# Optimization experiments

Measured on AMD Instinct MI355X. Metric: run time of the kernel, lower is better.

## Reference

```python
import jax, jax.numpy as jnp
import numpy as np

EPS = 1e-5
HEADS = 4
C = 128
GROUPS = 32  # min(32, 128//4)
SR = 2
SCALE = (C // HEADS) ** -0.5


def group_norm(x, gamma, beta, groups=GROUPS, eps=EPS):
    N, Ch, H, W = x.shape
    xg = x.reshape(N, groups, Ch // groups, H, W)
    mu = xg.mean(axis=(2, 3, 4), keepdims=True)
    var = xg.var(axis=(2, 3, 4), keepdims=True)
    xg = (xg - mu) * jax.lax.rsqrt(var + eps)
    x = xg.reshape(N, Ch, H, W)
    return x * gamma[None, :, None, None] + beta[None, :, None, None]


def conv1x1(x, W, b):
    # x: [N,C,H,W], W: [Cout,Cin], b: [Cout]
    return jnp.einsum('nchw,oc->nohw', x, W) + b[None, :, None, None]


def avg_pool2(x):
    N, Ch, H, W = x.shape
    return x.reshape(N, Ch, H // SR, SR, W // SR, SR).mean(axis=(3, 5))


def to_heads(x):
    # [N,C,H,W] -> [N,h,HW,C//h]  (matches view(N,h,C/h,HW).permute(0,1,3,2))
    N, Ch, H, W = x.shape
    return x.reshape(N, HEADS, Ch // HEADS, H * W).transpose(0, 1, 3, 2)


def setup_inputs() -> dict:
    key = jax.random.key(0)
    ks = jax.random.split(key, 16)
    B, H, W = 8, 64, 64
    s = 1.0 / np.sqrt(C)
    inp = {
        'q_src': jax.random.normal(ks[0], (B, C, H, W), jnp.float32),
        'k_src': jax.random.normal(ks[1], (B, C, H, W), jnp.float32),
        'v_src': jax.random.normal(ks[2], (B, C, H, W), jnp.float32),
        'Wq': jax.random.normal(ks[3], (C, C), jnp.float32) * s,
        'bq': jnp.zeros((C,), jnp.float32),
        'Wk': jax.random.normal(ks[4], (C, C), jnp.float32) * s,
        'bk': jnp.zeros((C,), jnp.float32),
        'Wv': jax.random.normal(ks[5], (C, C), jnp.float32) * s,
        'bv': jnp.zeros((C,), jnp.float32),
        'Wp': jax.random.normal(ks[6], (C, C), jnp.float32) * s,
        'bp': jnp.zeros((C,), jnp.float32),
        'g_nq': jnp.ones((C,), jnp.float32), 'b_nq': jnp.zeros((C,), jnp.float32),
        'g_nk': jnp.ones((C,), jnp.float32), 'b_nk': jnp.zeros((C,), jnp.float32),
        'g_nv': jnp.ones((C,), jnp.float32), 'b_nv': jnp.zeros((C,), jnp.float32),
        'g_srk': jnp.ones((C,), jnp.float32), 'b_srk': jnp.zeros((C,), jnp.float32),
        'g_srv': jnp.ones((C,), jnp.float32), 'b_srv': jnp.zeros((C,), jnp.float32),
    }
    return inp


def reference(q_src, k_src, v_src, Wq, bq, Wk, bk, Wv, bv, Wp, bp,
              g_nq, b_nq, g_nk, b_nk, g_nv, b_nv, g_srk, b_srk, g_srv, b_srv):
    # Q path: GN -> 1x1 conv
    q = conv1x1(group_norm(q_src, g_nq, b_nq), Wq, bq)
    # K/V paths: SR (avgpool + GN) -> GN -> 1x1 conv
    k = conv1x1(group_norm(group_norm(avg_pool2(k_src), g_srk, b_srk), g_nk, b_nk), Wk, bk)
    v = conv1x1(group_norm(group_norm(avg_pool2(v_src), g_srv, b_srv), g_nv, b_nv), Wv, bv)

    N, Cq, Hq, Wq_ = q.shape
    qh, kh, vh = to_heads(q), to_heads(k), to_heads(v)  # [N,h,L,d]
    attn = jnp.einsum('nhqd,nhkd->nhqk', qh * SCALE, kh)  # [N,h,Lq,Lk]
    attn = jax.nn.softmax(attn, axis=-1)
    out = jnp.einsum('nhqk,nhkd->nhqd', attn, vh)  # [N,h,Lq,d]
    out = out.transpose(0, 1, 3, 2).reshape(N, Cq, Hq, Wq_)
    return conv1x1(out, Wp, bp)
```

## Files before the change

### kernel.cpp

```cpp
#include <hip/hip_runtime.h>

typedef __attribute__((ext_vector_type(8)))  short s8v;
typedef __attribute__((ext_vector_type(4)))  short s4v;
typedef __attribute__((ext_vector_type(16))) float f16v;
typedef __attribute__((ext_vector_type(2)))  int   i2v;
typedef __attribute__((ext_vector_type(2)))  float f2v;

__device__ __forceinline__ unsigned short f2bf(float f) {
  union { float f; unsigned u; } v; v.f = f;
  unsigned r = v.u + 0x7FFFu + ((v.u >> 16) & 1u);
  return (unsigned short)(r >> 16);
}
__device__ __forceinline__ float bf2f(unsigned short b) {
  return __uint_as_float((unsigned)b << 16);
}
__device__ __forceinline__ float fexp2(float x) {
#if __has_builtin(__builtin_amdgcn_exp2f)
  return __builtin_amdgcn_exp2f(x);
#else
  return exp2f(x);
#endif
}
__device__ __forceinline__ f2v mk2(float a, float b) { f2v r; r[0] = a; r[1] = b; return r; }

__device__ __forceinline__ void gn_stats_body(
    int blk, const float* __restrict__ x, const float* __restrict__ gamma,
    const float* __restrict__ beta, float* __restrict__ ab, float* sh)
{
  int n = blk >> 5, g = blk & 31;
  int t = threadIdx.x; int cl = t >> 6, lane = t & 63;
  const float4* x4 = (const float4*)(x + (size_t)(n * 128 + g * 4 + cl) * 4096);
  float s = 0.f, ss = 0.f;
  #pragma unroll
  for (int j = 0; j < 16; ++j) {
    float4 v = x4[lane + 64 * j];
    s  += v.x + v.y + v.z + v.w;
    ss += v.x * v.x + v.y * v.y + v.z * v.z + v.w * v.w;
  }
  #pragma unroll
  for (int m = 32; m >= 1; m >>= 1) { s += __shfl_xor(s, m); ss += __shfl_xor(ss, m); }
  if (lane == 0) { sh[cl] = s; sh[4 + cl] = ss; }
  __syncthreads();
  if (t < 4) {
    float mu = (sh[0] + sh[1] + sh[2] + sh[3]) * (1.f / 16384.f);
    float e  = (sh[4] + sh[5] + sh[6] + sh[7]) * (1.f / 16384.f);
    float r  = rsqrtf(e - mu * mu + 1e-5f);
    int c = g * 4 + t;
    float al = gamma[c] * r;
    ab[n * 128 + c] = al;
    ab[1024 + n * 128 + c] = beta[c] - mu * al;
  }
}

__device__ __forceinline__ void pool_aff_body(
    int blk, const float* __restrict__ x,
    const float* __restrict__ g1, const float* __restrict__ b1,
    const float* __restrict__ g2, const float* __restrict__ b2,
    float* __restrict__ pooled, float* __restrict__ ab, float* sh)
{
  int n = blk >> 5, g = blk & 31;
  int t = threadIdx.x; int cl = t >> 6, lane = t & 63;
  int c = g * 4 + cl;
  const float* xb = x + (size_t)(n * 128 + c) * 4096;
  float* pb = pooled + (size_t)(n * 128 + c) * 1024;
  float s = 0.f, ss = 0.f;
  #pragma unroll
  for (int j = 0; j < 8; ++j) {
    int pp = (lane + 64 * j) * 2;
    int py = pp >> 5, px2 = pp & 31;
    const float* r0 = xb + py * 128 + px2 * 2;
    float4 A = *(const float4*)r0;
    float4 B = *(const float4*)(r0 + 64);
    float v0 = 0.25f * (A.x + A.y + B.x + B.y);
    float v1 = 0.25f * (A.z + A.w + B.z + B.w);
    float2 wv; wv.x = v0; wv.y = v1;
    *(float2*)(pb + pp) = wv;
    s += v0 + v1; ss += v0 * v0 + v1 * v1;
  }
  #pragma unroll
  for (int m = 32; m >= 1; m >>= 1) { s += __shfl_xor(s, m); ss += __shfl_xor(ss, m); }
  if (lane == 0) { sh[cl] = s; sh[4 + cl] = ss; }
  __syncthreads();
  if (t < 4) {
    float mu1 = (sh[0] + sh[1] + sh[2] + sh[3]) * (1.f / 4096.f);
    float e1  = (sh[4] + sh[5] + sh[6] + sh[7]) * (1.f / 4096.f);
    float r1  = rsqrtf(e1 - mu1 * mu1 + 1e-5f);
    float mzs = 0.f, e2s = 0.f;
    #pragma unroll
    for (int cc = 0; cc < 4; ++cc) {
      int ch = g * 4 + cc;
      float a = r1 * g1[ch];
      float d = b1[ch] - mu1 * a;
      float m = sh[cc] * (1.f / 1024.f);
      float q = sh[4 + cc] * (1.f / 1024.f);
      mzs += a * m + d;
      e2s += a * a * q + 2.f * a * d * m + d * d;
    }
    float mu2 = 0.25f * mzs;
    float r2  = rsqrtf(0.25f * e2s - mu2 * mu2 + 1e-5f);
    int ch = g * 4 + t;
    float a = r1 * g1[ch];
    float d = b1[ch] - mu1 * a;
    ab[n * 128 + ch] = a * r2 * g2[ch];
    ab[1024 + n * 128 + ch] = (d - mu2) * r2 * g2[ch] + b2[ch];
  }
}

__device__ __forceinline__ void wsplit_body(
    int b, const float* __restrict__ W, unsigned short* __restrict__ whi,
    unsigned short* __restrict__ wlo)
{
  int idx = b * 256 + threadIdx.x;
  #pragma unroll
  for (int k = 0; k < 4; ++k) {
    int f = idx + k * 4096;
    int o = f >> 7, c = f & 127;
    float v = W[f];
    unsigned short hb = f2bf(v);
    unsigned short lb = f2bf(v - bf2f(hb));
    int cq = c >> 2;
    int adr = (o * 16 + ((cq >> 1) ^ (o & 7))) * 8 + (cq & 1) * 4 + (c & 3);
    whi[adr] = hb; wlo[adr] = lb;
  }
}

__global__ __launch_bounds__(256) void prep_k(
    const float* __restrict__ q_src, const float* __restrict__ g_nq, const float* __restrict__ b_nq,
    const float* __restrict__ k_src, const float* __restrict__ g_srk, const float* __restrict__ b_srk,
    const float* __restrict__ g_nk, const float* __restrict__ b_nk,
    const float* __restrict__ v_src, const float* __restrict__ g_srv, const float* __restrict__ b_srv,
    const float* __restrict__ g_nv, const float* __restrict__ b_nv,
    const float* __restrict__ Wp,
    float* __restrict__ qab, float* __restrict__ kab, float* __restrict__ vab,
    float* __restrict__ knp, float* __restrict__ vnp,
    unsigned short* __restrict__ whi, unsigned short* __restrict__ wlo)
{
  __shared__ float sh[8];
  int b = blockIdx.x;
  if (b < 256) gn_stats_body(b, q_src, g_nq, b_nq, qab, sh);
  else if (b < 512) pool_aff_body(b - 256, k_src, g_srk, b_srk, g_nk, b_nk, knp, kab, sh);
  else if (b < 768) pool_aff_body(b - 512, v_src, g_srv, b_srv, g_nv, b_nv, vnp, vab, sh);
  else wsplit_body(b - 768, Wp, whi, wlo);
}

__device__ __forceinline__ void conv_body(
    int blk, const float* __restrict__ x, const float* __restrict__ ab,
    const float* __restrict__ W, const float* __restrict__ bias,
    unsigned short* __restrict__ po, int S, float outScale, int vt_mode,
    unsigned short* smem)
{
  unsigned short* Wsw = smem;
  unsigned short* xsw = smem + 16384;
  int t = threadIdx.x;
  int spb = S >> 7;
  int n  = blk / spb;
  int s0 = (blk % spb) << 7;

  #pragma unroll
  for (int k = 0; k < 16; ++k) {
    int f4 = t + (k << 8);
    int o = f4 >> 5, cq = f4 & 31;
    float4 wq = *(const float4*)(W + (size_t)o * 128 + cq * 4);
    union { unsigned q[2]; s4v v; } hv;
    asm("v_cvt_pk_bf16_f32 %0, %1, %2" : "=v"(hv.q[0]) : "v"(wq.x), "v"(wq.y));
    asm("v_cvt_pk_bf16_f32 %0, %1, %2" : "=v"(hv.q[1]) : "v"(wq.z), "v"(wq.w));
    *(s4v*)(Wsw + (o * 16 + ((cq >> 1) ^ (o & 7))) * 8 + (cq & 1) * 4) = hv.v;
  }
  int sl = t & 127, coh = t >> 7;
  for (int co = coh; co < 16; co += 2) {
    const float* xb = x + (size_t)(n * 128 + co * 8) * S + s0 + sl;
    const float* aa = ab + n * 128 + co * 8;
    const float* bb = aa + 1024;
    float f[8];
    #pragma unroll
    for (int e = 0; e < 8; ++e) f[e] = fmaf(xb[(size_t)e * S], aa[e], bb[e]);
    union { unsigned q[4]; s8v v; } xv;
    #pragma unroll
    for (int e = 0; e < 4; ++e)
      asm("v_cvt_pk_bf16_f32 %0, %1, %2" : "=v"(xv.q[e]) : "v"(f[2*e]), "v"(f[2*e+1]));
    *(s8v*)(xsw + (co * 128 + sl) * 8) = xv.v;
  }
  __syncthreads();

  int lane = t & 63, w = t >> 6;
  int l31 = lane & 31, h = lane >> 5;
  int wo = (w & 1) << 6, wsp = (w >> 1) << 6;
  f16v acc00 = {}, acc01 = {}, acc10 = {}, acc11 = {};
  #pragma unroll
  for (int reg = 0; reg < 16; ++reg) {
    int rm = (reg & 3) + ((reg >> 2) << 3) + (h << 2);
    float b0 = bias[wo + rm], b1 = bias[wo + 32 + rm];
    acc00[reg] = b0; acc01[reg] = b0; acc10[reg] = b1; acc11[reg] = b1;
  }
  const s8v* Wv = (const s8v*)Wsw;
  const s8v* Xv = (const s8v*)xsw;
  int o0 = wo + l31, o1 = wo + 32 + l31;
  #pragma unroll
  for (int cs = 0; cs < 8; ++cs) {
    int kk = cs * 2 + h;
    s8v a0 = Wv[o0 * 16 + (kk ^ (o0 & 7))];
    s8v a1 = Wv[o1 * 16 + (kk ^ (o1 & 7))];
    s8v b0 = Xv[kk * 128 + wsp + l31];
    s8v b1 = Xv[kk * 128 + wsp + 32 + l31];
    acc00 = __builtin_amdgcn_mfma_f32_32x32x16_bf16(a0, b0, acc00, 0, 0, 0);
    acc01 = __builtin_amdgcn_mfma_f32_32x32x16_bf16(a0, b1, acc01, 0, 0, 0);
    acc10 = __builtin_amdgcn_mfma_f32_32x32x16_bf16(a1, b0, acc10, 0, 0, 0);
    acc11 = __builtin_amdgcn_mfma_f32_32x32x16_bf16(a1, b1, acc11, 0, 0, 0);
  }
  __syncthreads();
  unsigned short* ot = smem;
  #pragma unroll
  for (int reg = 0; reg < 16; ++reg) {
    int rm = (reg & 3) + ((reg >> 2) << 3) + (h << 2);
    ot[(wo + rm) * 132 + wsp + l31]           = f2bf(acc00[reg] * outScale);
    ot[(wo + rm) * 132 + wsp + 32 + l31]      = f2bf(acc01[reg] * outScale);
    ot[(wo + 32 + rm) * 132 + wsp + l31]      = f2bf(acc10[reg] * outScale);
    ot[(wo + 32 + rm) * 132 + wsp + 32 + l31] = f2bf(acc11[reg] * outScale);
  }
  __syncthreads();
  if (!vt_mode) {
    unsigned* po32 = (unsigned*)po;
    int d2 = t & 15;
    for (int i = 0; i < 32; ++i) {
      int pr = (t >> 4) + (i << 4);
      int s = pr & 127, ohi_ = pr >> 7;
      unsigned lo = ot[(ohi_ * 32 + d2 * 2) * 132 + s];
      unsigned hi = ot[(ohi_ * 32 + d2 * 2 + 1) * 132 + s];
      po32[((size_t)(n * 4 + ohi_) * S + s0 + s) * 16 + d2] = lo | (hi << 16);
    }
  } else {
    unsigned* po32 = (unsigned*)po;
    const unsigned* ot32 = (const unsigned*)ot;
    int sp = t & 63;
    for (int i = 0; i < 32; ++i) {
      int rr = (t >> 6) + (i << 2);
      po32[((size_t)(n * 4 + (rr >> 5)) * 32 + (rr & 31)) * (S >> 1) + (s0 >> 1) + sp] =
          ot32[rr * 66 + sp];
    }
  }
}

__global__ __launch_bounds__(256) void convs_k(
    const float* __restrict__ q_src, const float* __restrict__ qab,
    const float* __restrict__ Wq, const float* __restrict__ bq, unsigned short* __restrict__ qhb,
    const float* __restrict__ knp, const float* __restrict__ kab,
    const float* __restrict__ Wk, const float* __restrict__ bk, unsigned short* __restrict__ khb,
    const float* __restrict__ vnp, const float* __restrict__ vab,
    const float* __restrict__ Wv, const float* __restrict__ bv, unsigned short* __restrict__ vtb,
    float qscale)
{
  __shared__ __align__(16) unsigned short smem[32768];
  int b = blockIdx.x;
  if (b < 256)      conv_body(b,       q_src, qab, Wq, bq, qhb, 4096, qscale, 0, smem);
  else if (b < 320) conv_body(b - 256, knp,   kab, Wk, bk, khb, 1024, 1.0f,   0, smem);
  else              conv_body(b - 320, vnp,   vab, Wv, bv, vtb, 1024, 1.0f,   1, smem);
}

__global__ __launch_bounds__(512, 4) void attn_proj_k(
    const unsigned short* __restrict__ qh, const unsigned short* __restrict__ kh,
    const unsigned short* __restrict__ vt, const unsigned short* __restrict__ whi,
    const unsigned short* __restrict__ wlo, const float* __restrict__ bp,
    float* __restrict__ out)
{
  __shared__ __align__(16) unsigned char SM[66560];
  unsigned short* S16 = (unsigned short*)SM;
  float* linvp = (float*)(SM + 65536);
  int t = threadIdx.x;
  int lane = t & 63, w = t >> 6;
  int l31 = lane & 31, h = lane >> 5;
  int hh = w & 3, qr = w >> 2;
  int blk = blockIdx.x;
  int n = blk >> 6, qb = blk & 63;

  const unsigned short* qp =
      qh + (((size_t)(n * 4 + hh) * 4096 + qb * 64 + qr * 32 + l31) << 5);
  s8v qf0 = *(const s8v*)(qp + h * 8);
  s8v qf1 = *(const s8v*)(qp + (2 + h) * 8);

  int sh_ = t >> 7, si = t & 127;
  size_t kvb = (size_t)(n * 4 + sh_) << 15;
  const unsigned short* kg = kh + kvb + ((si >> 2) << 5) + ((si & 3) << 3);
  const unsigned short* vg = vt + kvb + ((size_t)(si >> 3) << 10) + ((si & 7) << 3);
  int ku = (si & ~3) | ((si & 3) ^ ((si >> 3) & 3));
  int vu = (si & ~7) | ((si & 7) ^ ((si >> 3) & 7));

  s8v rk0 = *(const s8v*)kg;
  s8v rk1 = *(const s8v*)(kg + 1024);
  s8v rv0 = *(const s8v*)vg;
  s8v rv1 = *(const s8v*)(vg + 16384);
  {
    unsigned short* Kd = S16 + sh_ * 2048;
    unsigned short* Vd = S16 + 16384 + sh_ * 2048;
    *(s8v*)(Kd + ku * 8) = rk0;
    *(s8v*)(Kd + (ku + 128) * 8) = rk1;
    *(s8v*)(Vd + vu * 8) = rv0;
    *(s8v*)(Vd + (vu + 128) * 8) = rv1;
  }

  const f16v fz = {};
  f16v oacc = fz;
  f2v lp0 = mk2(0.f, 0.f), lp1 = mk2(0.f, 0.f);
  int kx = (l31 >> 1) & 3;
  int vx = l31 & 7;

  for (int tile = 0; tile < 16; ++tile) {
    int buf = tile & 1;
    __syncthreads();
    if (tile < 15) {
      int j = (tile + 1) << 6;
      rk0 = *(const s8v*)(kg + (size_t)j * 32);
      rk1 = *(const s8v*)(kg + (size_t)j * 32 + 1024);
      rv0 = *(const s8v*)(vg + j);
      rv1 = *(const s8v*)(vg + j + 16384);
    }
    const unsigned short* Kb = S16 + (buf * 4 + hh) * 2048;
    const unsigned short* Vb = S16 + 16384 + (buf * 4 + hh) * 2048;
    #pragma unroll
    for (int s = 0; s < 2; ++s) {
      int rb = s * 128 + l31 * 4;
      s8v kf0 = *(const s8v*)(Kb + ((rb + (h ^ kx)) << 3));
      s8v kf1 = *(const s8v*)(Kb + ((rb + ((2 + h) ^ kx)) << 3));
      __builtin_amdgcn_s_setprio(1);
      f16v sf = __builtin_amdgcn_mfma_f32_32x32x16_bf16(kf0, qf0, fz, 0, 0, 0);
      sf = __builtin_amdgcn_mfma_f32_32x32x16_bf16(kf1, qf1, sf, 0, 0, 0);
      __builtin_amdgcn_s_setprio(0);
      float p[16];
      #pragma unroll
      for (int r = 0; r < 16; ++r) p[r] = fexp2(sf[r]);
      lp0 += mk2(p[0], p[1]);  lp1 += mk2(p[2], p[3]);
      lp0 += mk2(p[4], p[5]);  lp1 += mk2(p[6], p[7]);
      lp0 += mk2(p[8], p[9]);  lp1 += mk2(p[10], p[11]);
      lp0 += mk2(p[12], p[13]); lp1 += mk2(p[14], p[15]);
      unsigned c[8];
      #pragma unroll
      for (int q = 0; q < 8; ++q)
        asm("v_cvt_pk_bf16_f32 %0, %1, %2" : "=v"(c[q]) : "v"(p[2 * q]), "v"(p[2 * q + 1]));
      i2v s02 = __builtin_amdgcn_permlane32_swap((int)c[0], (int)c[2], false, false);
      i2v s13 = __builtin_amdgcn_permlane32_swap((int)c[1], (int)c[3], false, false);
      i2v s46 = __builtin_amdgcn_permlane32_swap((int)c[4], (int)c[6], false, false);
      i2v s57 = __builtin_amdgcn_permlane32_swap((int)c[5], (int)c[7], false, false);
      union { int u[4]; s8v v; } u0, u1;
      u0.u[0] = s02[0]; u0.u[1] = s13[0]; u0.u[2] = s02[1]; u0.u[3] = s13[1];
      u1.u[0] = s46[0]; u1.u[1] = s57[0]; u1.u[2] = s46[1]; u1.u[3] = s57[1];
      s8v vf0 = *(const s8v*)(Vb + ((l31 * 8 + ((s * 4 + h) ^ vx)) << 3));
      s8v vf1 = *(const s8v*)(Vb + ((l31 * 8 + ((s * 4 + 2 + h) ^ vx)) << 3));
      __builtin_amdgcn_s_setprio(1);
      oacc = __builtin_amdgcn_mfma_f32_32x32x16_bf16(u0.v, vf0, oacc, 0, 0, 0);
      oacc = __builtin_amdgcn_mfma_f32_32x32x16_bf16(u1.v, vf1, oacc, 0, 0, 0);
      __builtin_amdgcn_s_setprio(0);
    }
    if (tile < 15) {
      unsigned short* Kd = S16 + ((buf ^ 1) * 4 + sh_) * 2048;
      unsigned short* Vd = S16 + 16384 + ((buf ^ 1) * 4 + sh_) * 2048;
      *(s8v*)(Kd + ku * 8) = rk0;
      *(s8v*)(Kd + (ku + 128) * 8) = rk1;
      *(s8v*)(Vd + vu * 8) = rv0;
      *(s8v*)(Vd + (vu + 128) * 8) = rv1;
    }
  }

  float l_part = lp0[0] + lp0[1] + lp1[0] + lp1[1];
  float l_tot = l_part + __shfl_xor(l_part, 32);
  if (h == 0) linvp[hh * 64 + qr * 32 + l31] = 1.0f / l_tot;
  __syncthreads();

  unsigned short* Xh16 = S16;
  unsigned short* Xl16 = S16 + 16384;
  int ch = hh * 32 + l31, co = ch >> 3, el = ch & 7;
  #pragma unroll
  for (int reg = 0; reg < 16; ++reg) {
    int rm = (reg & 3) + ((reg >> 2) << 3) + (h << 2);
    int row = qr * 32 + rm;
    float val = oacc[reg] * linvp[hh * 64 + row];
    unsigned short hb = f2bf(val);
    unsigned short lb = f2bf(val - bf2f(hb));
    int xu = co * 64 + (row ^ co);
    Xh16[xu * 8 + el] = hb;
    Xl16[xu * 8 + el] = lb;
  }
  __syncthreads();

  int ol = hh * 32 + l31;
  const s8v* WH = (const s8v*)whi;
  const s8v* WL = (const s8v*)wlo;
  s8v ah[8], al[8];
  #pragma unroll
  for (int cs = 0; cs < 8; ++cs) {
    int kk = cs * 2 + h;
    int ia = ol * 16 + (kk ^ (ol & 7));
    ah[cs] = WH[ia];
    al[cs] = WL[ia];
  }
  f16v acc;
  #pragma unroll
  for (int reg = 0; reg < 16; ++reg) {
    int rm = (reg & 3) + ((reg >> 2) << 3) + (h << 2);
    acc[reg] = bp[hh * 32 + rm];
  }
  int srow = qr * 32 + l31;
  #pragma unroll
  for (int cs = 0; cs < 8; ++cs) {
    int kk = cs * 2 + h;
    int xu = kk * 64 + (srow ^ kk);
    s8v bh = *(const s8v*)(Xh16 + xu * 8);
    s8v bl = *(const s8v*)(Xl16 + xu * 8);
    acc = __builtin_amdgcn_mfma_f32_32x32x16_bf16(ah[cs], bh, acc, 0, 0, 0);
    acc = __builtin_amdgcn_mfma_f32_32x32x16_bf16(ah[cs], bl, acc, 0, 0, 0);
    acc = __builtin_amdgcn_mfma_f32_32x32x16_bf16(al[cs], bh, acc, 0, 0, 0);
  }
  #pragma unroll
  for (int reg = 0; reg < 16; ++reg) {
    int rm = (reg & 3) + ((reg >> 2) << 3) + (h << 2);
    out[(size_t)(n * 128 + hh * 32 + rm) * 4096 + qb * 64 + srow] = acc[reg];
  }
}

extern "C" void kernel_launch(void* const* d_in, const int* in_sizes, int n_in,
                              void* d_out, int out_size, void* d_ws, size_t ws_size,
                              hipStream_t stream)
{
  (void)in_sizes; (void)n_in; (void)out_size; (void)ws_size;
  const float* q_src = (const float*)d_in[0];
  const float* k_src = (const float*)d_in[1];
  const float* v_src = (const float*)d_in[2];
  const float* Wq = (const float*)d_in[3];
  const float* bq = (const float*)d_in[4];
  const float* Wk = (const float*)d_in[5];
  const float* bk = (const float*)d_in[6];
  const float* Wv = (const float*)d_in[7];
  const float* bv = (const float*)d_in[8];
  const float* Wp = (const float*)d_in[9];
  const float* bp = (const float*)d_in[10];
  const float* g_nq  = (const float*)d_in[11];
  const float* b_nq  = (const float*)d_in[12];
  const float* g_nk  = (const float*)d_in[13];
  const float* b_nk  = (const float*)d_in[14];
  const float* g_nv  = (const float*)d_in[15];
  const float* b_nv  = (const float*)d_in[16];
  const float* g_srk = (const float*)d_in[17];
  const float* b_srk = (const float*)d_in[18];
  const float* g_srv = (const float*)d_in[19];
  const float* b_srv = (const float*)d_in[20];

  unsigned short* qhb = (unsigned short*)d_ws;
  unsigned short* khb = qhb + 4194304;
  unsigned short* vtb = khb + 1048576;
  float* knp  = (float*)(vtb + 1048576);
  float* vnp  = knp + 1048576;
  float* qab  = vnp + 1048576;
  float* kab  = qab + 2048;
  float* vab  = kab + 2048;
  unsigned short* whi = (unsigned short*)(vab + 2048);
  unsigned short* wlo = whi + 16384;

  const float QSCALE = 0.17677669529663688f * 1.44269504088896340f;

  prep_k<<<784, 256, 0, stream>>>(q_src, g_nq, b_nq,
                                  k_src, g_srk, b_srk, g_nk, b_nk,
                                  v_src, g_srv, b_srv, g_nv, b_nv,
                                  Wp, qab, kab, vab, knp, vnp, whi, wlo);
  convs_k<<<384, 256, 0, stream>>>(q_src, qab, Wq, bq, qhb,
                                   knp, kab, Wk, bk, khb,
                                   vnp, vab, Wv, bv, vtb, QSCALE);
  attn_proj_k<<<512, 512, 0, stream>>>(qhb, khb, vtb, whi, wlo, bp, (float*)d_out);
}
```

Before: 65.32 us.

## Load K/V fragments straight from global memory and remap blocks per XCD

The attention kernel no longer stages K and V tiles through double-buffered LDS with per-tile barriers. Each wave now reads its MFMA K/V fragments directly from global memory inside a fully unrolled loop. This removes the barriers and LDS traffic, and the smaller shared footprint should allow higher occupancy. Block indices are also remapped so that every block of a given batch lands on the same XCD, which keeps its K/V in that XCD's L2. The cost is more global/L2 load traffic: waves that share a head fetch the same K/V separately, and load latency is now exposed without explicit prefetching.

```diff
diff --git a/kernel.cpp b/kernel.cpp
--- a/kernel.cpp
+++ b/kernel.cpp
@@ -262,14 +262,15 @@
     const unsigned short* __restrict__ wlo, const float* __restrict__ bp,
     float* __restrict__ out)
 {
-  __shared__ __align__(16) unsigned char SM[66560];
-  unsigned short* S16 = (unsigned short*)SM;
-  float* linvp = (float*)(SM + 65536);
+  __shared__ __align__(16) unsigned short Xh16[8192];
+  __shared__ __align__(16) unsigned short Xl16[8192];
+  __shared__ float linvp[256];
   int t = threadIdx.x;
   int lane = t & 63, w = t >> 6;
   int l31 = lane & 31, h = lane >> 5;
   int hh = w & 3, qr = w >> 2;
-  int blk = blockIdx.x;
+  int b0 = blockIdx.x;
+  int blk = (b0 & 7) * 64 + (b0 >> 3);
   int n = blk >> 6, qb = blk & 63;
 
   const unsigned short* qp =
@@ -277,49 +278,23 @@
   s8v qf0 = *(const s8v*)(qp + h * 8);
   s8v qf1 = *(const s8v*)(qp + (2 + h) * 8);
 
-  int sh_ = t >> 7, si = t & 127;
-  size_t kvb = (size_t)(n * 4 + sh_) << 15;
-  const unsigned short* kg = kh + kvb + ((si >> 2) << 5) + ((si & 3) << 3);
-  const unsigned short* vg = vt + kvb + ((size_t)(si >> 3) << 10) + ((si & 7) << 3);
-  int ku = (si & ~3) | ((si & 3) ^ ((si >> 3) & 3));
-  int vu = (si & ~7) | ((si & 7) ^ ((si >> 3) & 7));
-
-  s8v rk0 = *(const s8v*)kg;
-  s8v rk1 = *(const s8v*)(kg + 1024);
-  s8v rv0 = *(const s8v*)vg;
-  s8v rv1 = *(const s8v*)(vg + 16384);
-  {
-    unsigned short* Kd = S16 + sh_ * 2048;
-    unsigned short* Vd = S16 + 16384 + sh_ * 2048;
-    *(s8v*)(Kd + ku * 8) = rk0;
-    *(s8v*)(Kd + (ku + 128) * 8) = rk1;
-    *(s8v*)(Vd + vu * 8) = rv0;
-    *(s8v*)(Vd + (vu + 128) * 8) = rv1;
-  }
+  size_t kvb = (size_t)(n * 4 + hh) << 15;
+  const unsigned short* kp = kh + kvb + (l31 << 5) + h * 8;
+  const unsigned short* vp = vt + kvb + ((size_t)l31 << 10) + h * 8;
 
   const f16v fz = {};
   f16v oacc = fz;
   f2v lp0 = mk2(0.f, 0.f), lp1 = mk2(0.f, 0.f);
-  int kx = (l31 >> 1) & 3;
-  int vx = l31 & 7;
-
+
+  #pragma unroll
   for (int tile = 0; tile < 16; ++tile) {
-    int buf = tile & 1;
-    __syncthreads();
-    if (tile < 15) {
-      int j = (tile + 1) << 6;
-      rk0 = *(const s8v*)(kg + (size_t)j * 32);
-      rk1 = *(const s8v*)(kg + (size_t)j * 32 + 1024);
-      rv0 = *(const s8v*)(vg + j);
-      rv1 = *(const s8v*)(vg + j + 16384);
-    }
-    const unsigned short* Kb = S16 + (buf * 4 + hh) * 2048;
-    const unsigned short* Vb = S16 + 16384 + (buf * 4 + hh) * 2048;
     #pragma unroll
     for (int s = 0; s < 2; ++s) {
-      int rb = s * 128 + l31 * 4;
-      s8v kf0 = *(const s8v*)(Kb + ((rb + (h ^ kx)) << 3));
-      s8v kf1 = *(const s8v*)(Kb + ((rb + ((2 + h) ^ kx)) << 3));
+      int off = (tile << 6) + (s << 5);
+      s8v kf0 = *(const s8v*)(kp + off * 32);
+      s8v kf1 = *(const s8v*)(kp + off * 32 + 16);
+      s8v vf0 = *(const s8v*)(vp + off);
+      s8v vf1 = *(const s8v*)(vp + off + 16);
       __builtin_amdgcn_s_setprio(1);
       f16v sf = __builtin_amdgcn_mfma_f32_32x32x16_bf16(kf0, qf0, fz, 0, 0, 0);
       sf = __builtin_amdgcn_mfma_f32_32x32x16_bf16(kf1, qf1, sf, 0, 0, 0);
@@ -342,30 +317,17 @@
       union { int u[4]; s8v v; } u0, u1;
       u0.u[0] = s02[0]; u0.u[1] = s13[0]; u0.u[2] = s02[1]; u0.u[3] = s13[1];
       u1.u[0] = s46[0]; u1.u[1] = s57[0]; u1.u[2] = s46[1]; u1.u[3] = s57[1];
-      s8v vf0 = *(const s8v*)(Vb + ((l31 * 8 + ((s * 4 + h) ^ vx)) << 3));
-      s8v vf1 = *(const s8v*)(Vb + ((l31 * 8 + ((s * 4 + 2 + h) ^ vx)) << 3));
       __builtin_amdgcn_s_setprio(1);
       oacc = __builtin_amdgcn_mfma_f32_32x32x16_bf16(u0.v, vf0, oacc, 0, 0, 0);
       oacc = __builtin_amdgcn_mfma_f32_32x32x16_bf16(u1.v, vf1, oacc, 0, 0, 0);
       __builtin_amdgcn_s_setprio(0);
     }
-    if (tile < 15) {
-      unsigned short* Kd = S16 + ((buf ^ 1) * 4 + sh_) * 2048;
-      unsigned short* Vd = S16 + 16384 + ((buf ^ 1) * 4 + sh_) * 2048;
-      *(s8v*)(Kd + ku * 8) = rk0;
-      *(s8v*)(Kd + (ku + 128) * 8) = rk1;
-      *(s8v*)(Vd + vu * 8) = rv0;
-      *(s8v*)(Vd + (vu + 128) * 8) = rv1;
-    }
   }
 
   float l_part = lp0[0] + lp0[1] + lp1[0] + lp1[1];
   float l_tot = l_part + __shfl_xor(l_part, 32);
   if (h == 0) linvp[hh * 64 + qr * 32 + l31] = 1.0f / l_tot;
-  __syncthreads();
-
-  unsigned short* Xh16 = S16;
-  unsigned short* Xl16 = S16 + 16384;
+
   int ch = hh * 32 + l31, co = ch >> 3, el = ch & 7;
   #pragma unroll
   for (int reg = 0; reg < 16; ++reg) {
```

Result: slower. 80.35 us (+23.0%).
